# Kernel optimization log

Hardware: AMD Instinct MI355X
Metric: run time of the kernel (lower is better)

## Reference

```python
import jax, jax.numpy as jnp
import numpy as np

IN_FEATURE = 4096
OUT_FEATURE = 4096
BLOCK_SIZE = 128
NUM_BLOCKS = IN_FEATURE // BLOCK_SIZE


def setup_inputs() -> dict:
    key = jax.random.key(0)
    k1, k2 = jax.random.split(key)
    x = jax.random.normal(k1, (4, 2048, IN_FEATURE), dtype=jnp.float32)
    # weight laid out as the original nn.Linear: [out_feature, in_feature]
    weight = jax.random.normal(k2, (OUT_FEATURE, IN_FEATURE), dtype=jnp.float32) * (1.0 / np.sqrt(IN_FEATURE))
    return {"x": x, "weight": weight}


def reference(x, weight):
    # The grouped 1x1 conv + reduce-sum over blocks is exactly a blockwise
    # matmul summed over blocks, i.e. out = x @ weight.T.
    # Expressed per-block to mirror the original structure without the
    # conv/permute/reshape overhead:
    b, s, in_f = x.shape
    xb = x.reshape(b, s, NUM_BLOCKS, BLOCK_SIZE)            # [b,s,nb,k]
    wb = weight.reshape(OUT_FEATURE, NUM_BLOCKS, BLOCK_SIZE)  # [o,nb,k]
    # sum over blocks (nb) and block_size (k) == full contraction over in_feature
    out = jnp.einsum('bsnk,onk->bso', xb, wb)
    return out
```

## Files before the change

kernel.cpp:

```cpp
#include <hip/hip_runtime.h>
#include <hip/hip_bf16.h>
#include <stdint.h>


typedef __bf16 bf16x8 __attribute__((ext_vector_type(8)));
typedef float f32x4 __attribute__((ext_vector_type(4)));
typedef float f32x16 __attribute__((ext_vector_type(16)));

__device__ __forceinline__ unsigned short f2bf(float f) {
  unsigned u = __builtin_bit_cast(unsigned, f);
  u += 0x7FFFu + ((u >> 16) & 1u);
  return (unsigned short)(u >> 16);
}

__global__ void cvt_f32_to_bf16(const float* __restrict__ src,
                                unsigned short* __restrict__ dst, long n4) {
  long i = (long)blockIdx.x * blockDim.x + threadIdx.x;
  const long stride = (long)gridDim.x * blockDim.x;
  for (; i < n4; i += stride) {
    float4 v = reinterpret_cast<const float4*>(src)[i];
    ushort4 o;
    o.x = f2bf(v.x); o.y = f2bf(v.y); o.z = f2bf(v.z); o.w = f2bf(v.w);
    reinterpret_cast<ushort4*>(dst)[i] = o;
  }
}

__device__ __forceinline__ void gload_lds16(const void* g, void* lds) {
  __builtin_amdgcn_global_load_lds(
      (__attribute__((address_space(1))) void*)(g),
      (__attribute__((address_space(3))) void*)(lds), 16, 0, 0);
}

#define BARRIER()                                    \
  do {                                               \
    asm volatile("" ::: "memory");                   \
    __builtin_amdgcn_s_barrier();                    \
    asm volatile("" ::: "memory");                   \
  } while (0)
#define WAIT_VM4() asm volatile("s_waitcnt vmcnt(4)" ::: "memory")
#define WAIT_VM0() asm volatile("s_waitcnt vmcnt(0)" ::: "memory")

#define READ_A(AB, P)                                                        \
  _Pragma("unroll") for (int mi = 0; mi < 2; ++mi) {                         \
    const int row_ = ((P)*2 + mi) * 32 + l31;                                \
    _Pragma("unroll") for (int ks = 0; ks < 4; ++ks)                         \
        fa[(P)*2 + mi][ks] =                                                 \
            *(const bf16x8*)((AB) + row_ * 128 + ((kq + ks * 32) ^ xc));     \
  }
#define READ_B(BB, NI)                                                       \
  {                                                                          \
    const int row_ = brow0 + (NI)*32 + l31;                                  \
    _Pragma("unroll") for (int ks = 0; ks < 4; ++ks)                         \
        fb[NI][ks] =                                                         \
            *(const bf16x8*)((BB) + row_ * 128 + ((kq + ks * 32) ^ xc));     \
  }
#define MQ(P, NI)                                                            \
  _Pragma("unroll") for (int ks = 0; ks < 4; ++ks)                           \
  _Pragma("unroll") for (int mi = 0; mi < 2; ++mi)                           \
      acc[(P)*2 + mi][NI] = __builtin_amdgcn_mfma_f32_32x32x16_bf16(         \
          fa[(P)*2 + mi][ks], fb[NI][ks], acc[(P)*2 + mi][NI], 0, 0, 0);

#define PH(READS, STAGES, MQCALL, WAITS)  \
  do {                                    \
    READS STAGES BARRIER();               \
    __builtin_amdgcn_s_setprio(1);        \
    MQCALL                                \
    __builtin_amdgcn_s_setprio(0);        \
    WAITS BARRIER();                      \
  } while (0)

__global__ __launch_bounds__(512, 2) void gemm256(
    const unsigned short* __restrict__ A, const unsigned short* __restrict__ B,
    float* __restrict__ C, int M, int N, int K) {
  __shared__ __attribute__((aligned(1024))) char lds[131072];
  const int A00 = 0, A01 = 16384, A10 = 32768, A11 = 49152;
  const int B00 = 65536, B01 = 81920, B10 = 98304, B11 = 114688;

  const int t = threadIdx.x;
  const int l = t & 63;
  const int w = t >> 6;
  const int wm = w >> 2;
  const int wn = w & 3;
  const int l31 = l & 31;
  const int kq = (l >> 5) * 16;
  const int xc = (l & 7) << 4;
  const int brow0 = (wn & 1) * 64;
  const int srow = l >> 3;
  const int sslot = ((l & 7) ^ ((l >> 3) & 7)) * 8;

  const int nwg = gridDim.x;
  int swz = blockIdx.x;
  if ((nwg & 7) == 0) swz = (swz & 7) * (nwg >> 3) + (swz >> 3);
  const int ntx = N >> 8;
  const int bx = swz % ntx;
  const int by = swz / ntx;
  const int mBase = by * 256, nBase = bx * 256;

  const char* Ard0 = lds + wm * 16384;
  const char* Ard1 = lds + 32768 + wm * 16384;
  const char* Brd0 = lds + 65536 + (wn >> 1) * 16384;
  const char* Brd1 = lds + 98304 + (wn >> 1) * 16384;

  bf16x8 fa[4][2 * 2], fb[2][4];
  f32x16 acc[4][2] = {};

  auto STAGE = [&](const unsigned short* __restrict__ G, int row0, int k0,
                   int ldsOff) {
    const unsigned short* s =
        G + (size_t)(row0 + w * 8 + srow) * K + k0 + sslot;
    char* d = lds + ldsOff + w * 1024;
    gload_lds16(s, d);
    gload_lds16(s + (size_t)64 * K, d + 8192);
  };

  STAGE(A, mBase, 0, A00);
  STAGE(A, mBase + 128, 0, A01);
  STAGE(B, nBase, 0, B00);
  STAGE(B, nBase + 128, 0, B01);
  STAGE(B, nBase, 64, B10);
  STAGE(A, mBase, 64, A10);
  WAIT_VM4();
  BARRIER();

  const int itermain = K / 128 - 1;
  for (int i = 0; i < itermain; ++i) {
    const int kA = (2 * i + 1) * 64;
    const int kB = kA + 64;
    const int kC = kB + 64;
    PH(READ_A(Ard0, 0) READ_B(Brd0, 0), STAGE(A, mBase + 128, kA, A11);, MQ(0, 0), );
    PH(READ_B(Brd0, 1),                 STAGE(B, nBase + 128, kA, B11);, MQ(0, 1), );
    PH(READ_A(Ard0, 1),                 STAGE(B, nBase,       kB, B00);, MQ(1, 0), );
    PH(,                                STAGE(A, mBase,       kB, A00);, MQ(1, 1), WAIT_VM4(););
    PH(READ_A(Ard1, 0) READ_B(Brd1, 0), STAGE(A, mBase + 128, kB, A01);, MQ(0, 0), );
    PH(READ_B(Brd1, 1),                 STAGE(B, nBase + 128, kB, B01);, MQ(0, 1), );
    PH(READ_A(Ard1, 1),                 STAGE(B, nBase,       kC, B10);, MQ(1, 0), );
    PH(,                                STAGE(A, mBase,       kC, A10);, MQ(1, 1), WAIT_VM4(););
  }

  {
    const int kT = K - 64;
    PH(READ_A(Ard0, 0) READ_B(Brd0, 0), STAGE(A, mBase + 128, kT, A11);, MQ(0, 0), );
    PH(READ_B(Brd0, 1),                 STAGE(B, nBase + 128, kT, B11);, MQ(0, 1), );
    PH(READ_A(Ard0, 1),                 ,                                MQ(1, 0), );
    PH(,                                ,                                MQ(1, 1), WAIT_VM0(););
    PH(READ_A(Ard1, 0) READ_B(Brd1, 0), ,                                MQ(0, 0), );
    PH(READ_B(Brd1, 1),                 ,                                MQ(0, 1), );
    PH(READ_A(Ard1, 1),                 ,                                MQ(1, 0), );
    PH(,                                ,                                MQ(1, 1), );
  }

  const int cl = l & 31, ch = l >> 5;
  float* Cw = C + (size_t)(mBase + wm * 128 + 4 * ch) * N + nBase + wn * 64 + cl;
#pragma unroll
  for (int mi = 0; mi < 4; ++mi)
#pragma unroll
    for (int ni = 0; ni < 2; ++ni)
#pragma unroll
      for (int r = 0; r < 16; ++r)
        Cw[(size_t)(mi * 32 + (r & 3) + 8 * (r >> 2)) * N + ni * 32] =
            acc[mi][ni][r];
}

typedef unsigned short ushort8f __attribute__((ext_vector_type(8)));
__global__ __launch_bounds__(256) void gemm_fb(
    const float* __restrict__ Af, const float* __restrict__ Wf,
    float* __restrict__ C, int M, int N, int K) {
  __shared__ __attribute__((aligned(16))) unsigned short Ash[128 * 64];
  __shared__ __attribute__((aligned(16))) unsigned short Bsh[128 * 64];
  const int t = threadIdx.x, l = t & 63, w = t >> 6;
  const int mBase = blockIdx.y * 128, nBase = blockIdx.x * 128;
  const int wm = w >> 1, wn = w & 1;
  const int lr = l & 15, lk = (l >> 4) * 8;
  f32x4 acc[4][4] = {};
  const int frow = t >> 1, fkh = (t & 1) * 32;
  for (int k0 = 0; k0 < K; k0 += 64) {
    const float* ga = Af + (size_t)(mBase + frow) * K + k0 + fkh;
    const float* gb = Wf + (size_t)(nBase + frow) * K + k0 + fkh;
#pragma unroll
    for (int j = 0; j < 4; ++j) {
      float4 a0 = reinterpret_cast<const float4*>(ga)[2 * j];
      float4 a1 = reinterpret_cast<const float4*>(ga)[2 * j + 1];
      float4 b0 = reinterpret_cast<const float4*>(gb)[2 * j];
      float4 b1 = reinterpret_cast<const float4*>(gb)[2 * j + 1];
      ushort8f oa = {f2bf(a0.x), f2bf(a0.y), f2bf(a0.z), f2bf(a0.w),
                     f2bf(a1.x), f2bf(a1.y), f2bf(a1.z), f2bf(a1.w)};
      ushort8f ob = {f2bf(b0.x), f2bf(b0.y), f2bf(b0.z), f2bf(b0.w),
                     f2bf(b1.x), f2bf(b1.y), f2bf(b1.z), f2bf(b1.w)};
      *reinterpret_cast<ushort8f*>(&Ash[frow * 64 + fkh + j * 8]) = oa;
      *reinterpret_cast<ushort8f*>(&Bsh[frow * 64 + fkh + j * 8]) = ob;
    }
    __syncthreads();
#pragma unroll
    for (int kk = 0; kk < 2; ++kk) {
      bf16x8 a[4], b[4];
#pragma unroll
      for (int mi = 0; mi < 4; ++mi)
        a[mi] = *reinterpret_cast<const bf16x8*>(
            &Ash[(wm * 64 + mi * 16 + lr) * 64 + kk * 32 + lk]);
#pragma unroll
      for (int ni = 0; ni < 4; ++ni)
        b[ni] = *reinterpret_cast<const bf16x8*>(
            &Bsh[(wn * 64 + ni * 16 + lr) * 64 + kk * 32 + lk]);
#pragma unroll
      for (int mi = 0; mi < 4; ++mi)
#pragma unroll
        for (int ni = 0; ni < 4; ++ni)
          acc[mi][ni] = __builtin_amdgcn_mfma_f32_16x16x32_bf16(
              a[mi], b[ni], acc[mi][ni], 0, 0, 0);
    }
    __syncthreads();
  }
  const int crow0 = mBase + wm * 64 + (l >> 4) * 4;
  const int ccol0 = nBase + wn * 64 + lr;
#pragma unroll
  for (int mi = 0; mi < 4; ++mi)
#pragma unroll
    for (int ni = 0; ni < 4; ++ni)
#pragma unroll
      for (int r = 0; r < 4; ++r)
        C[(size_t)(crow0 + mi * 16 + r) * N + ccol0 + ni * 16] =
            acc[mi][ni][r];
}

extern "C" void kernel_launch(void* const* d_in, const int* in_sizes, int n_in,
                              void* d_out, int out_size, void* d_ws, size_t ws_size,
                              hipStream_t stream) {
  (void)n_in; (void)out_size;
  const float* x = (const float*)d_in[0];
  const float* wgt = (const float*)d_in[1];
  float* out = (float*)d_out;

  const long x_elems = in_sizes[0];
  const long w_elems = in_sizes[1];
  const int K = 4096;
  const int M = (int)(x_elems / K);
  const int N = (int)(w_elems / K);

  const size_t need = (size_t)(x_elems + w_elems) * sizeof(unsigned short);
  const bool ok256 =
      (M % 256 == 0) && (N % 256 == 0) && (K % 128 == 0) && (K >= 256) &&
      ws_size >= need;
  if (ok256) {
    unsigned short* Abf = (unsigned short*)d_ws;
    unsigned short* Wbf = Abf + x_elems;
    cvt_f32_to_bf16<<<2048, 256, 0, stream>>>(x, Abf, x_elems / 4);
    cvt_f32_to_bf16<<<2048, 256, 0, stream>>>(wgt, Wbf, w_elems / 4);
    gemm256<<<dim3((M / 256) * (N / 256)), 512, 0, stream>>>(Abf, Wbf, out, M,
                                                             N, K);
  } else {
    dim3 grid(N / 128, M / 128);
    gemm_fb<<<grid, 256, 0, stream>>>(x, wgt, out, M, N, K);
  }
}
```

Baseline: 309.2 us.

## Rearrange LDS tile layout and reorder MFMA phases to drop one barrier per phase

Changes the global-to-LDS staging pattern so each wave writes 8 rows by 8 k-slots in a layout that fragment reads can index with constant offsets, replacing the XOR swizzle. MFMA phases now split over k-halves (2 m x 2 n x 2 k) instead of over n columns, with A/B fragment reads grouped to match. The barrier between the reads and the MFMAs in each phase is removed, leaving one barrier per phase, and the final phase's trailing barrier is dropped. This cuts synchronization and address arithmetic, but the new LDS layout may bring bank conflicts, and removing the barrier relies on the remaining barriers to keep LDS reads and the async stage writes correctly ordered.

```diff
diff --git a/kernel.cpp b/kernel.cpp
--- a/kernel.cpp
+++ b/kernel.cpp
@@ -40,31 +40,32 @@
 #define WAIT_VM4() asm volatile("s_waitcnt vmcnt(4)" ::: "memory")
 #define WAIT_VM0() asm volatile("s_waitcnt vmcnt(0)" ::: "memory")
 
-#define READ_A(AB, P)                                                        \
-  _Pragma("unroll") for (int mi = 0; mi < 2; ++mi) {                         \
-    const int row_ = ((P)*2 + mi) * 32 + l31;                                \
-    _Pragma("unroll") for (int ks = 0; ks < 4; ++ks)                         \
-        fa[(P)*2 + mi][ks] =                                                 \
-            *(const bf16x8*)((AB) + row_ * 128 + ((kq + ks * 32) ^ xc));     \
-  }
-#define READ_B(BB, NI)                                                       \
-  {                                                                          \
-    const int row_ = brow0 + (NI)*32 + l31;                                  \
-    _Pragma("unroll") for (int ks = 0; ks < 4; ++ks)                         \
-        fb[NI][ks] =                                                         \
-            *(const bf16x8*)((BB) + row_ * 128 + ((kq + ks * 32) ^ xc));     \
-  }
-#define MQ(P, NI)                                                            \
-  _Pragma("unroll") for (int ks = 0; ks < 4; ++ks)                           \
+#define RDA(AB, MI, KS)                                                      \
+  fa[MI][KS] = *(const bf16x8*)((AB) + (MI)*4096 + (KS)*256 + abase);
+#define RDB(BB, NI, KS)                                                      \
+  fb[NI][KS] = *(const bf16x8*)((BB) + (NI)*4096 + (KS)*256 + bbase);
+#define READ_P1(AB, BB)                                                      \
+  RDA(AB, 0, 0) RDA(AB, 0, 1) RDA(AB, 1, 0) RDA(AB, 1, 1)                    \
+  RDB(BB, 0, 0) RDB(BB, 0, 1) RDB(BB, 1, 0) RDB(BB, 1, 1)
+#define READ_P2(AB, BB)                                                      \
+  RDA(AB, 0, 2) RDA(AB, 0, 3) RDA(AB, 1, 2) RDA(AB, 1, 3)                    \
+  RDB(BB, 0, 2) RDB(BB, 0, 3) RDB(BB, 1, 2) RDB(BB, 1, 3)
+#define READ_P3(AB)                                                          \
+  RDA(AB, 2, 0) RDA(AB, 2, 1) RDA(AB, 2, 2) RDA(AB, 2, 3)                    \
+  RDA(AB, 3, 0) RDA(AB, 3, 1) RDA(AB, 3, 2) RDA(AB, 3, 3)
+#define MQ32(M0, K0)                                                         \
+  _Pragma("unroll") for (int kx = 0; kx < 2; ++kx)                           \
   _Pragma("unroll") for (int mi = 0; mi < 2; ++mi)                           \
-      acc[(P)*2 + mi][NI] = __builtin_amdgcn_mfma_f32_32x32x16_bf16(         \
-          fa[(P)*2 + mi][ks], fb[NI][ks], acc[(P)*2 + mi][NI], 0, 0, 0);
-
-#define PH(READS, STAGES, MQCALL, WAITS)  \
+  _Pragma("unroll") for (int ni = 0; ni < 2; ++ni)                           \
+      acc[(M0) + mi][ni] = __builtin_amdgcn_mfma_f32_32x32x16_bf16(          \
+          fa[(M0) + mi][(K0) + kx], fb[ni][(K0) + kx], acc[(M0) + mi][ni],   \
+          0, 0, 0);
+
+#define PH(READS, STAGES, MQS, WAITS)     \
   do {                                    \
-    READS STAGES BARRIER();               \
+    READS STAGES                          \
     __builtin_amdgcn_s_setprio(1);        \
-    MQCALL                                \
+    MQS                                   \
     __builtin_amdgcn_s_setprio(0);        \
     WAITS BARRIER();                      \
   } while (0)
@@ -82,11 +83,10 @@
   const int wm = w >> 2;
   const int wn = w & 3;
   const int l31 = l & 31;
-  const int kq = (l >> 5) * 16;
-  const int xc = (l & 7) << 4;
-  const int brow0 = (wn & 1) * 64;
-  const int srow = l >> 3;
-  const int sslot = ((l & 7) ^ ((l >> 3) & 7)) * 8;
+  const int abase = (l31 >> 3) * 1024 + (l >> 5) * 128 + (l31 & 7) * 16;
+  const int bbase = (wn & 1) * 8192 + abase;
+  const int srow = l & 7;
+  const int sslot = (l >> 3) * 8;
 
   const int nwg = gridDim.x;
   int swz = blockIdx.x;
@@ -101,7 +101,7 @@
   const char* Brd0 = lds + 65536 + (wn >> 1) * 16384;
   const char* Brd1 = lds + 98304 + (wn >> 1) * 16384;
 
-  bf16x8 fa[4][2 * 2], fb[2][4];
+  bf16x8 fa[4][4], fb[2][4];
   f32x16 acc[4][2] = {};
 
   auto STAGE = [&](const unsigned short* __restrict__ G, int row0, int k0,
@@ -127,26 +127,28 @@
     const int kA = (2 * i + 1) * 64;
     const int kB = kA + 64;
     const int kC = kB + 64;
-    PH(READ_A(Ard0, 0) READ_B(Brd0, 0), STAGE(A, mBase + 128, kA, A11);, MQ(0, 0), );
-    PH(READ_B(Brd0, 1),                 STAGE(B, nBase + 128, kA, B11);, MQ(0, 1), );
-    PH(READ_A(Ard0, 1),                 STAGE(B, nBase,       kB, B00);, MQ(1, 0), );
-    PH(,                                STAGE(A, mBase,       kB, A00);, MQ(1, 1), WAIT_VM4(););
-    PH(READ_A(Ard1, 0) READ_B(Brd1, 0), STAGE(A, mBase + 128, kB, A01);, MQ(0, 0), );
-    PH(READ_B(Brd1, 1),                 STAGE(B, nBase + 128, kB, B01);, MQ(0, 1), );
-    PH(READ_A(Ard1, 1),                 STAGE(B, nBase,       kC, B10);, MQ(1, 0), );
-    PH(,                                STAGE(A, mBase,       kC, A10);, MQ(1, 1), WAIT_VM4(););
+    PH(READ_P1(Ard0, Brd0), STAGE(A, mBase + 128, kA, A11);, MQ32(0, 0), );
+    PH(READ_P2(Ard0, Brd0), STAGE(B, nBase + 128, kA, B11);, MQ32(0, 2), );
+    PH(READ_P3(Ard0),       STAGE(B, nBase,       kB, B00);, MQ32(2, 0), );
+    PH(,                    STAGE(A, mBase,       kB, A00);, MQ32(2, 2), WAIT_VM4(););
+    PH(READ_P1(Ard1, Brd1), STAGE(A, mBase + 128, kB, A01);, MQ32(0, 0), );
+    PH(READ_P2(Ard1, Brd1), STAGE(B, nBase + 128, kB, B01);, MQ32(0, 2), );
+    PH(READ_P3(Ard1),       STAGE(B, nBase,       kC, B10);, MQ32(2, 0), );
+    PH(,                    STAGE(A, mBase,       kC, A10);, MQ32(2, 2), WAIT_VM4(););
   }
 
   {
     const int kT = K - 64;
-    PH(READ_A(Ard0, 0) READ_B(Brd0, 0), STAGE(A, mBase + 128, kT, A11);, MQ(0, 0), );
-    PH(READ_B(Brd0, 1),                 STAGE(B, nBase + 128, kT, B11);, MQ(0, 1), );
-    PH(READ_A(Ard0, 1),                 ,                                MQ(1, 0), );
-    PH(,                                ,                                MQ(1, 1), WAIT_VM0(););
-    PH(READ_A(Ard1, 0) READ_B(Brd1, 0), ,                                MQ(0, 0), );
-    PH(READ_B(Brd1, 1),                 ,                                MQ(0, 1), );
-    PH(READ_A(Ard1, 1),                 ,                                MQ(1, 0), );
-    PH(,                                ,                                MQ(1, 1), );
+    PH(READ_P1(Ard0, Brd0), STAGE(A, mBase + 128, kT, A11);, MQ32(0, 0), );
+    PH(READ_P2(Ard0, Brd0), STAGE(B, nBase + 128, kT, B11);, MQ32(0, 2), );
+    PH(READ_P3(Ard0),       ,                                MQ32(2, 0), );
+    PH(,                    ,                                MQ32(2, 2), WAIT_VM0(););
+    PH(READ_P1(Ard1, Brd1), ,                                MQ32(0, 0), );
+    PH(READ_P2(Ard1, Brd1), ,                                MQ32(0, 2), );
+    PH(READ_P3(Ard1),       ,                                MQ32(2, 0), );
+    __builtin_amdgcn_s_setprio(1);
+    MQ32(2, 2)
+    __builtin_amdgcn_s_setprio(0);
   }
 
   const int cl = l & 31, ch = l >> 5;
```

Result: slower. 325.7 us (+5.3%).
